# Kernel optimization log

Measured on AMD Instinct MI355X. Metric: run time of the kernel, lower is better.

The kernel has to match this reference:

```python
import jax, jax.numpy as jnp
import numpy as np

N = 6144      # nodes
NFEAT = 512
NHID = 256
NHEADS = 4
DHEAD = NHID // NHEADS  # 64
NEMBED = 128
NEG_INF = -9e15
LRELU_ALPHA = 0.2


def setup_inputs() -> dict:
    key = jax.random.key(0)
    k = jax.random.split(key, 8)
    x = jax.random.normal(k[0], (N, NFEAT), dtype=jnp.float32)
    adj = (jax.random.uniform(k[1], (N, N)) < 0.01).astype(jnp.int32)
    # per-head GAT params, packed over heads
    W = jax.random.normal(k[2], (NHEADS, NFEAT, DHEAD), dtype=jnp.float32) * 0.05
    a_src = jax.random.normal(k[3], (NHEADS, DHEAD), dtype=jnp.float32) * 0.05
    a_dst = jax.random.normal(k[4], (NHEADS, DHEAD), dtype=jnp.float32) * 0.05
    # output linear (init.normal_ std=0.05 per reset_parameters)
    lin_w = jax.random.normal(k[5], (NEMBED, NHID), dtype=jnp.float32) * 0.05
    lin_b = jnp.zeros((NEMBED,), dtype=jnp.float32)
    return {"x": x, "adj": adj, "W": W, "a_src": a_src, "a_dst": a_dst,
            "lin_w": lin_w, "lin_b": lin_b}


def _gat_forward(x, adj, W, a_src, a_dst, lin_w, lin_b):
    # Wh: [H, N, D]
    Wh = jnp.einsum('nf,hfd->hnd', x, W)
    # attention logits e_ij = leakyrelu(a_src.Wh_i + a_dst.Wh_j): [H, N, N]
    s = jnp.einsum('hnd,hd->hn', Wh, a_src)   # source term per node
    t = jnp.einsum('hnd,hd->hn', Wh, a_dst)   # target term per node
    e = s[:, :, None] + t[:, None, :]
    e = jax.nn.leaky_relu(e, negative_slope=LRELU_ALPHA)
    # mask by adjacency, softmax over neighbors
    e = jnp.where(adj[None, :, :] > 0, e, NEG_INF)
    attn = jax.nn.softmax(e, axis=-1)
    # aggregate and per-head ELU (concat=True GAT layer)
    h = jnp.einsum('hnm,hmd->hnd', attn, Wh)
    h = jax.nn.elu(h)
    # concat heads -> [N, NHID]
    h = jnp.transpose(h, (1, 0, 2)).reshape(N, NHID)
    # dropout is identity in eval mode; linear + ELU
    out = jax.nn.elu(h @ lin_w.T + lin_b)
    return out


def reference(x, adj, W, a_src, a_dst, lin_w, lin_b):
    return _gat_forward(x, adj, W, a_src, a_dst, lin_w, lin_b)
```

## Files before the change

### kernel.cpp

```cpp
#include <hip/hip_runtime.h>
#include <hip/hip_bf16.h>
#include <math.h>

#define N_NODES 6144
#define NFEAT 512
#define NHID 256
#define NHEADS 4
#define DHEAD 64
#define NEMBED 128
#define LRELU_ALPHA 0.2f
#define MAXC 256
#define ASTRIDE 20

static __device__ __forceinline__ unsigned short f2bf(float f) {
    unsigned u = __float_as_uint(f);
    unsigned r = (u + 0x7FFFu + ((u >> 16) & 1u)) >> 16;
    return (unsigned short)r;
}

__global__ __launch_bounds__(256) void gemm_scan(const float* __restrict__ x,
                                                 const float* __restrict__ W,
                                                 const float* __restrict__ a_src,
                                                 const float* __restrict__ a_dst,
                                                 const int* __restrict__ adj,
                                                 unsigned short* __restrict__ Whb,
                                                 float* __restrict__ s_arr,
                                                 float* __restrict__ t_arr,
                                                 int* __restrict__ cnt_g,
                                                 unsigned short* __restrict__ nbr_g) {
    __shared__ float As[64][ASTRIDE];
    __shared__ float Bs[16][64];
    const int tid = threadIdx.x;

    if (blockIdx.y < NHEADS) {
        const int tx = tid & 15;
        const int ty = tid >> 4;
        const int row0 = blockIdx.x * 64;
        const int h = blockIdx.y;
        const float* Bp = W + (size_t)h * NFEAT * DHEAD;

        float acc[4][4] = {};

        for (int k0 = 0; k0 < NFEAT; k0 += 16) {
            {
                const int r = tid >> 2, kq = tid & 3;
                const float4 v = *(const float4*)(x + (size_t)(row0 + r) * NFEAT + k0 + kq * 4);
                *(float4*)&As[r][kq * 4] = v;
            }
            {
                const int kk = tid >> 4, cq = tid & 15;
                const float4 v = *(const float4*)(Bp + (size_t)(k0 + kk) * DHEAD + cq * 4);
                *(float4*)&Bs[kk][cq * 4] = v;
            }
            __syncthreads();
#pragma unroll
            for (int kk = 0; kk < 16; kk++) {
                float a[4], b[4];
#pragma unroll
                for (int i = 0; i < 4; i++) a[i] = As[ty * 4 + i][kk];
#pragma unroll
                for (int j = 0; j < 4; j++) b[j] = Bs[kk][tx * 4 + j];
#pragma unroll
                for (int i = 0; i < 4; i++)
#pragma unroll
                    for (int j = 0; j < 4; j++) acc[i][j] += a[i] * b[j];
            }
            __syncthreads();
        }
#pragma unroll
        for (int i = 0; i < 4; i++) {
            const int row = row0 + ty * 4 + i;
            ushort4 w;
            w.x = f2bf(acc[i][0]);
            w.y = f2bf(acc[i][1]);
            w.z = f2bf(acc[i][2]);
            w.w = f2bf(acc[i][3]);
            *(ushort4*)(Whb + ((size_t)h * N_NODES + row) * DHEAD + tx * 4) = w;
        }
        float a4s[4], a4d[4];
#pragma unroll
        for (int j = 0; j < 4; j++) {
            a4s[j] = a_src[h * DHEAD + tx * 4 + j];
            a4d[j] = a_dst[h * DHEAD + tx * 4 + j];
        }
#pragma unroll
        for (int i = 0; i < 4; i++) {
            float ps = acc[i][0] * a4s[0] + acc[i][1] * a4s[1] +
                       acc[i][2] * a4s[2] + acc[i][3] * a4s[3];
            float pt = acc[i][0] * a4d[0] + acc[i][1] * a4d[1] +
                       acc[i][2] * a4d[2] + acc[i][3] * a4d[3];
#pragma unroll
            for (int off = 1; off < 16; off <<= 1) {
                ps += __shfl_xor(ps, off);
                pt += __shfl_xor(pt, off);
            }
            if (tx == 0) {
                const int row = row0 + ty * 4 + i;
                s_arr[h * N_NODES + row] = ps;
                t_arr[h * N_NODES + row] = pt;
            }
        }
    } else {
        const int r = (blockIdx.y - NHEADS) * gridDim.x + blockIdx.x;
        const int* arow = adj + (size_t)r * N_NODES;
        unsigned short* nrow = nbr_g + (size_t)r * MAXC;
        int* cp = cnt_g + r;
#pragma unroll
        for (int it = 0; it < 6; ++it) {
            const int j0 = it * 1024 + tid * 4;
            const int4 v = *(const int4*)(arow + j0);
            const int n = (v.x != 0) + (v.y != 0) + (v.z != 0) + (v.w != 0);
            if (n) {
                int base = atomicAdd(cp, n);
                if (v.x) { if (base < MAXC) nrow[base] = (unsigned short)j0; ++base; }
                if (v.y) { if (base < MAXC) nrow[base] = (unsigned short)(j0 + 1); ++base; }
                if (v.z) { if (base < MAXC) nrow[base] = (unsigned short)(j0 + 2); ++base; }
                if (v.w) { if (base < MAXC) nrow[base] = (unsigned short)(j0 + 3); }
            }
        }
    }
}

__global__ __launch_bounds__(256) void attn_agg(const int* __restrict__ adj,
                                                const unsigned short* __restrict__ Whb,
                                                const float* __restrict__ s_arr,
                                                const float* __restrict__ t_arr,
                                                const int* __restrict__ cnt_g,
                                                const unsigned short* __restrict__ nbr_g,
                                                float* __restrict__ hcat) {
    __shared__ unsigned short nbr[MAXC];
    __shared__ float p_s[NHEADS][MAXC];
    const int i = blockIdx.x;
    const int tid = threadIdx.x;
    const int h = tid >> 6;
    const int lane = tid & 63;
    const int half = lane >> 5;
    const int dp = (lane & 31) * 2;
    const int c = cnt_g[i];
    const unsigned short* wp = Whb + (size_t)h * N_NODES * DHEAD;

    float r0 = 0.0f, r1 = 0.0f, l = 1.0f;
    bool combine = true;
    if (c > 0 && c <= MAXC) {
        for (int k = tid; k < c; k += 256) nbr[k] = nbr_g[(size_t)i * MAXC + k];
        __syncthreads();

        const float s_h = s_arr[h * N_NODES + i];
        const float* tp = t_arr + (size_t)h * N_NODES;
        float m = -INFINITY;
        for (int k = lane; k < c; k += 64) {
            float e = s_h + tp[nbr[k]];
            e = e >= 0.0f ? e : LRELU_ALPHA * e;
            p_s[h][k] = e;
            m = fmaxf(m, e);
        }
#pragma unroll
        for (int off = 32; off > 0; off >>= 1) m = fmaxf(m, __shfl_xor(m, off));
        float ls = 0.0f;
        for (int k = lane; k < c; k += 64) {
            const float p = __expf(p_s[h][k] - m);
            p_s[h][k] = p;
            ls += p;
        }
#pragma unroll
        for (int off = 32; off > 0; off >>= 1) ls += __shfl_xor(ls, off);
        l = ls;

        float ax[8] = {0.f, 0.f, 0.f, 0.f, 0.f, 0.f, 0.f, 0.f};
        float ay[8] = {0.f, 0.f, 0.f, 0.f, 0.f, 0.f, 0.f, 0.f};
        int k = 0;
        for (; k + 16 <= c; k += 16) {
#pragma unroll
            for (int s2 = 0; s2 < 8; ++s2) {
                const int kk = k + 2 * s2 + half;
                const int j = nbr[kk];
                const float p = p_s[h][kk];
                const unsigned w = *(const unsigned*)(wp + (size_t)j * DHEAD + dp);
                ax[s2] += p * __uint_as_float(w << 16);
                ay[s2] += p * __uint_as_float(w & 0xffff0000u);
            }
        }
        for (; k < c; k += 2) {
            const int kk = k + half;
            int j = nbr[k];
            float p = 0.0f;
            if (kk < c) { j = nbr[kk]; p = p_s[h][kk]; }
            const unsigned w = *(const unsigned*)(wp + (size_t)j * DHEAD + dp);
            ax[0] += p * __uint_as_float(w << 16);
            ay[0] += p * __uint_as_float(w & 0xffff0000u);
        }
        r0 = ((ax[0] + ax[1]) + (ax[2] + ax[3])) + ((ax[4] + ax[5]) + (ax[6] + ax[7]));
        r1 = ((ay[0] + ay[1]) + (ay[2] + ay[3])) + ((ay[4] + ay[5]) + (ay[6] + ay[7]));
    } else if (c == 0) {
        for (int j = half; j < N_NODES; j += 2) {
            const unsigned w = *(const unsigned*)(wp + (size_t)j * DHEAD + dp);
            r0 += __uint_as_float(w << 16);
            r1 += __uint_as_float(w & 0xffff0000u);
        }
        l = (float)N_NODES;
    } else {
        combine = false;
        const int* arow = adj + (size_t)i * N_NODES;
        const float s_h = s_arr[h * N_NODES + i];
        const float* tp = t_arr + (size_t)h * N_NODES;
        float m = -INFINITY, ll = 0.0f;
        for (int j = 0; j < N_NODES; j++) {
            if (arow[j]) {
                float e = s_h + tp[j];
                e = e >= 0.0f ? e : LRELU_ALPHA * e;
                const float m_new = fmaxf(m, e);
                const float scale = __expf(m - m_new);
                const float p = __expf(e - m_new);
                ll = ll * scale + p;
                const unsigned w = *(const unsigned*)(wp + (size_t)j * DHEAD + dp);
                r0 = r0 * scale + p * __uint_as_float(w << 16);
                r1 = r1 * scale + p * __uint_as_float(w & 0xffff0000u);
                m = m_new;
            }
        }
        l = ll;
    }
    if (combine) {
        r0 += __shfl_xor(r0, 32);
        r1 += __shfl_xor(r1, 32);
    }
    float hx = r0 / l, hy = r1 / l;
    hx = hx > 0.0f ? hx : expm1f(hx);
    hy = hy > 0.0f ? hy : expm1f(hy);
    if (lane < 32) {
        *(float2*)(hcat + (size_t)i * NHID + h * DHEAD + dp) = make_float2(hx, hy);
    }
}

__global__ __launch_bounds__(256) void out_gemm(const float* __restrict__ hcat,
                                                const float* __restrict__ lin_w,
                                                const float* __restrict__ lin_b,
                                                float* __restrict__ out) {
    __shared__ float As[64][ASTRIDE * 4];
    __shared__ float Bs[16][64];
    const int tid = threadIdx.x;
    const int tx = tid & 15;
    const int ty = tid >> 4;
    const int row0 = blockIdx.x * 64;
    const int c0 = blockIdx.y * 64;

    float acc[4][4] = {};

    for (int k0 = 0; k0 < NHID; k0 += 16) {
        {
            const int r = tid >> 2, kq = tid & 3;
            const float4 v = *(const float4*)(hcat + (size_t)(row0 + r) * NHID + k0 + kq * 4);
            *(float4*)&As[r][kq * 4] = v;
        }
        {
            const int cc = tid & 63, kq = tid >> 6;
            const float4 v = *(const float4*)(lin_w + (size_t)(c0 + cc) * NHID + k0 + kq * 4);
            Bs[kq * 4 + 0][cc] = v.x;
            Bs[kq * 4 + 1][cc] = v.y;
            Bs[kq * 4 + 2][cc] = v.z;
            Bs[kq * 4 + 3][cc] = v.w;
        }
        __syncthreads();
#pragma unroll
        for (int kk = 0; kk < 16; kk++) {
            float a[4], b[4];
#pragma unroll
            for (int i = 0; i < 4; i++) a[i] = As[ty * 4 + i][kk];
#pragma unroll
            for (int j = 0; j < 4; j++) b[j] = Bs[kk][tx * 4 + j];
#pragma unroll
            for (int i = 0; i < 4; i++)
#pragma unroll
                for (int j = 0; j < 4; j++) acc[i][j] += a[i] * b[j];
        }
        __syncthreads();
    }
#pragma unroll
    for (int i = 0; i < 4; i++) {
        const int row = row0 + ty * 4 + i;
        float v[4];
#pragma unroll
        for (int j = 0; j < 4; j++) {
            const int col = c0 + tx * 4 + j;
            float val = acc[i][j] + lin_b[col];
            v[j] = val > 0.0f ? val : expm1f(val);
        }
        *(float4*)(out + (size_t)row * NEMBED + c0 + tx * 4) =
            make_float4(v[0], v[1], v[2], v[3]);
    }
}

extern "C" void kernel_launch(void* const* d_in, const int* in_sizes, int n_in,
                              void* d_out, int out_size, void* d_ws, size_t ws_size,
                              hipStream_t stream) {
    const float* x     = (const float*)d_in[0];
    const int*   adj   = (const int*)d_in[1];
    const float* W     = (const float*)d_in[2];
    const float* a_src = (const float*)d_in[3];
    const float* a_dst = (const float*)d_in[4];
    const float* lin_w = (const float*)d_in[5];
    const float* lin_b = (const float*)d_in[6];
    float* out = (float*)d_out;

    unsigned short* Whb = (unsigned short*)d_ws;
    float* s    = (float*)(Whb + (size_t)NHEADS * N_NODES * DHEAD);
    float* t    = s + (size_t)NHEADS * N_NODES;
    float* hcat = t + (size_t)NHEADS * N_NODES;
    int* cnt_g  = (int*)(hcat + (size_t)N_NODES * NHID);
    unsigned short* nbr_g = (unsigned short*)(cnt_g + N_NODES);

    hipMemsetAsync(cnt_g, 0, N_NODES * sizeof(int), stream);
    gemm_scan<<<dim3(96, NHEADS + 64), 256, 0, stream>>>(
        x, W, a_src, a_dst, adj, Whb, s, t, cnt_g, nbr_g);
    attn_agg<<<N_NODES, 256, 0, stream>>>(adj, Whb, s, t, cnt_g, nbr_g, hcat);
    out_gemm<<<dim3(N_NODES / 64, NEMBED / 64), 256, 0, stream>>>(hcat, lin_w, lin_b, out);
}
```

Measured before the change: 277.9 us.

## Fuse output linear into attention kernel and count neighbors in LDS

The output linear layer plus ELU is folded into the per-node attention kernel. Each block writes its concatenated hidden row to shared memory and computes the 128 outputs with wave-level dot products against lin_w. This removes the hcat round trip through global memory and one kernel launch. The neighbor scan now counts in a shared-memory atomic and writes the count once, which drops the memset and the global atomics. Aggregation now uses 8-byte bf16 loads with four neighbors in flight per wave. The cost is that every block rereads lin_w (128 KB) from cache, and a serial per-row dot-product loop is added.

```diff
diff --git a/kernel.cpp b/kernel.cpp
--- a/kernel.cpp
+++ b/kernel.cpp
@@ -17,6 +17,8 @@
     unsigned r = (u + 0x7FFFu + ((u >> 16) & 1u)) >> 16;
     return (unsigned short)r;
 }
+static __device__ __forceinline__ float bfLo(unsigned u) { return __uint_as_float(u << 16); }
+static __device__ __forceinline__ float bfHi(unsigned u) { return __uint_as_float(u & 0xffff0000u); }
 
 __global__ __launch_bounds__(256) void gemm_scan(const float* __restrict__ x,
                                                  const float* __restrict__ W,
@@ -30,6 +32,7 @@
                                                  unsigned short* __restrict__ nbr_g) {
     __shared__ float As[64][ASTRIDE];
     __shared__ float Bs[16][64];
+    __shared__ int scnt;
     const int tid = threadIdx.x;
 
     if (blockIdx.y < NHEADS) {
@@ -104,43 +107,52 @@
         const int r = (blockIdx.y - NHEADS) * gridDim.x + blockIdx.x;
         const int* arow = adj + (size_t)r * N_NODES;
         unsigned short* nrow = nbr_g + (size_t)r * MAXC;
-        int* cp = cnt_g + r;
+        if (tid == 0) scnt = 0;
+        __syncthreads();
 #pragma unroll
         for (int it = 0; it < 6; ++it) {
             const int j0 = it * 1024 + tid * 4;
             const int4 v = *(const int4*)(arow + j0);
             const int n = (v.x != 0) + (v.y != 0) + (v.z != 0) + (v.w != 0);
             if (n) {
-                int base = atomicAdd(cp, n);
+                int base = atomicAdd(&scnt, n);
                 if (v.x) { if (base < MAXC) nrow[base] = (unsigned short)j0; ++base; }
                 if (v.y) { if (base < MAXC) nrow[base] = (unsigned short)(j0 + 1); ++base; }
                 if (v.z) { if (base < MAXC) nrow[base] = (unsigned short)(j0 + 2); ++base; }
                 if (v.w) { if (base < MAXC) nrow[base] = (unsigned short)(j0 + 3); }
             }
         }
+        __syncthreads();
+        if (tid == 0) cnt_g[r] = scnt;
     }
 }
 
-__global__ __launch_bounds__(256) void attn_agg(const int* __restrict__ adj,
+__global__ __launch_bounds__(256) void attn_out(const int* __restrict__ adj,
                                                 const unsigned short* __restrict__ Whb,
                                                 const float* __restrict__ s_arr,
                                                 const float* __restrict__ t_arr,
                                                 const int* __restrict__ cnt_g,
                                                 const unsigned short* __restrict__ nbr_g,
-                                                float* __restrict__ hcat) {
+                                                const float* __restrict__ lin_w,
+                                                const float* __restrict__ lin_b,
+                                                float* __restrict__ out) {
     __shared__ unsigned short nbr[MAXC];
     __shared__ float p_s[NHEADS][MAXC];
+    __shared__ float hrow[NHID];
+    __shared__ float part[NEMBED];
     const int i = blockIdx.x;
     const int tid = threadIdx.x;
     const int h = tid >> 6;
     const int lane = tid & 63;
-    const int half = lane >> 5;
-    const int dp = (lane & 31) * 2;
+    const int q = lane >> 4;
+    const int dq = (lane & 15) * 4;
     const int c = cnt_g[i];
     const unsigned short* wp = Whb + (size_t)h * N_NODES * DHEAD;
 
-    float r0 = 0.0f, r1 = 0.0f, l = 1.0f;
+    float b0[4] = {0.f, 0.f, 0.f, 0.f};
+    float l = 1.0f;
     bool combine = true;
+
     if (c > 0 && c <= MAXC) {
         for (int k = tid; k < c; k += 256) nbr[k] = nbr_g[(size_t)i * MAXC + k];
         __syncthreads();
@@ -166,36 +178,43 @@
         for (int off = 32; off > 0; off >>= 1) ls += __shfl_xor(ls, off);
         l = ls;
 
-        float ax[8] = {0.f, 0.f, 0.f, 0.f, 0.f, 0.f, 0.f, 0.f};
-        float ay[8] = {0.f, 0.f, 0.f, 0.f, 0.f, 0.f, 0.f, 0.f};
+        float b1[4] = {0.f, 0.f, 0.f, 0.f};
+        float b2[4] = {0.f, 0.f, 0.f, 0.f};
+        float b3[4] = {0.f, 0.f, 0.f, 0.f};
         int k = 0;
         for (; k + 16 <= c; k += 16) {
-#pragma unroll
-            for (int s2 = 0; s2 < 8; ++s2) {
-                const int kk = k + 2 * s2 + half;
-                const int j = nbr[kk];
-                const float p = p_s[h][kk];
-                const unsigned w = *(const unsigned*)(wp + (size_t)j * DHEAD + dp);
-                ax[s2] += p * __uint_as_float(w << 16);
-                ay[s2] += p * __uint_as_float(w & 0xffff0000u);
-            }
-        }
-        for (; k < c; k += 2) {
-            const int kk = k + half;
-            int j = nbr[k];
-            float p = 0.0f;
-            if (kk < c) { j = nbr[kk]; p = p_s[h][kk]; }
-            const unsigned w = *(const unsigned*)(wp + (size_t)j * DHEAD + dp);
-            ax[0] += p * __uint_as_float(w << 16);
-            ay[0] += p * __uint_as_float(w & 0xffff0000u);
-        }
-        r0 = ((ax[0] + ax[1]) + (ax[2] + ax[3])) + ((ax[4] + ax[5]) + (ax[6] + ax[7]));
-        r1 = ((ay[0] + ay[1]) + (ay[2] + ay[3])) + ((ay[4] + ay[5]) + (ay[6] + ay[7]));
+            const int k0 = k + q, k1 = k + 4 + q, k2 = k + 8 + q, k3 = k + 12 + q;
+            const int j0 = nbr[k0], j1 = nbr[k1], j2 = nbr[k2], j3 = nbr[k3];
+            const float p0 = p_s[h][k0], p1 = p_s[h][k1];
+            const float p2 = p_s[h][k2], p3 = p_s[h][k3];
+            const uint2 w0 = *(const uint2*)(wp + (size_t)j0 * DHEAD + dq);
+            const uint2 w1 = *(const uint2*)(wp + (size_t)j1 * DHEAD + dq);
+            const uint2 w2 = *(const uint2*)(wp + (size_t)j2 * DHEAD + dq);
+            const uint2 w3 = *(const uint2*)(wp + (size_t)j3 * DHEAD + dq);
+            b0[0] += p0 * bfLo(w0.x); b0[1] += p0 * bfHi(w0.x);
+            b0[2] += p0 * bfLo(w0.y); b0[3] += p0 * bfHi(w0.y);
+            b1[0] += p1 * bfLo(w1.x); b1[1] += p1 * bfHi(w1.x);
+            b1[2] += p1 * bfLo(w1.y); b1[3] += p1 * bfHi(w1.y);
+            b2[0] += p2 * bfLo(w2.x); b2[1] += p2 * bfHi(w2.x);
+            b2[2] += p2 * bfLo(w2.y); b2[3] += p2 * bfHi(w2.y);
+            b3[0] += p3 * bfLo(w3.x); b3[1] += p3 * bfHi(w3.x);
+            b3[2] += p3 * bfLo(w3.y); b3[3] += p3 * bfHi(w3.y);
+        }
+        for (; k < c; k += 4) {
+            const int kk = k + q;
+            const int j = (kk < c) ? nbr[kk] : nbr[k];
+            const float p = (kk < c) ? p_s[h][kk] : 0.0f;
+            const uint2 w = *(const uint2*)(wp + (size_t)j * DHEAD + dq);
+            b0[0] += p * bfLo(w.x); b0[1] += p * bfHi(w.x);
+            b0[2] += p * bfLo(w.y); b0[3] += p * bfHi(w.y);
+        }
+#pragma unroll
+        for (int d = 0; d < 4; d++) b0[d] = (b0[d] + b1[d]) + (b2[d] + b3[d]);
     } else if (c == 0) {
-        for (int j = half; j < N_NODES; j += 2) {
-            const unsigned w = *(const unsigned*)(wp + (size_t)j * DHEAD + dp);
-            r0 += __uint_as_float(w << 16);
-            r1 += __uint_as_float(w & 0xffff0000u);
+        for (int j = q; j < N_NODES; j += 4) {
+            const uint2 w = *(const uint2*)(wp + (size_t)j * DHEAD + dq);
+            b0[0] += bfLo(w.x); b0[1] += bfHi(w.x);
+            b0[2] += bfLo(w.y); b0[3] += bfHi(w.y);
         }
         l = (float)N_NODES;
     } else {
@@ -212,82 +231,49 @@
                 const float scale = __expf(m - m_new);
                 const float p = __expf(e - m_new);
                 ll = ll * scale + p;
-                const unsigned w = *(const unsigned*)(wp + (size_t)j * DHEAD + dp);
-                r0 = r0 * scale + p * __uint_as_float(w << 16);
-                r1 = r1 * scale + p * __uint_as_float(w & 0xffff0000u);
+                const uint2 w = *(const uint2*)(wp + (size_t)j * DHEAD + dq);
+                b0[0] = b0[0] * scale + p * bfLo(w.x);
+                b0[1] = b0[1] * scale + p * bfHi(w.x);
+                b0[2] = b0[2] * scale + p * bfLo(w.y);
+                b0[3] = b0[3] * scale + p * bfHi(w.y);
                 m = m_new;
             }
         }
         l = ll;
     }
+
     if (combine) {
-        r0 += __shfl_xor(r0, 32);
-        r1 += __shfl_xor(r1, 32);
-    }
-    float hx = r0 / l, hy = r1 / l;
-    hx = hx > 0.0f ? hx : expm1f(hx);
-    hy = hy > 0.0f ? hy : expm1f(hy);
-    if (lane < 32) {
-        *(float2*)(hcat + (size_t)i * NHID + h * DHEAD + dp) = make_float2(hx, hy);
-    }
-}
-
-__global__ __launch_bounds__(256) void out_gemm(const float* __restrict__ hcat,
-                                                const float* __restrict__ lin_w,
-                                                const float* __restrict__ lin_b,
-                                                float* __restrict__ out) {
-    __shared__ float As[64][ASTRIDE * 4];
-    __shared__ float Bs[16][64];
-    const int tid = threadIdx.x;
-    const int tx = tid & 15;
-    const int ty = tid >> 4;
-    const int row0 = blockIdx.x * 64;
-    const int c0 = blockIdx.y * 64;
-
-    float acc[4][4] = {};
-
-    for (int k0 = 0; k0 < NHID; k0 += 16) {
-        {
-            const int r = tid >> 2, kq = tid & 3;
-            const float4 v = *(const float4*)(hcat + (size_t)(row0 + r) * NHID + k0 + kq * 4);
-            *(float4*)&As[r][kq * 4] = v;
-        }
-        {
-            const int cc = tid & 63, kq = tid >> 6;
-            const float4 v = *(const float4*)(lin_w + (size_t)(c0 + cc) * NHID + k0 + kq * 4);
-            Bs[kq * 4 + 0][cc] = v.x;
-            Bs[kq * 4 + 1][cc] = v.y;
-            Bs[kq * 4 + 2][cc] = v.z;
-            Bs[kq * 4 + 3][cc] = v.w;
-        }
-        __syncthreads();
-#pragma unroll
-        for (int kk = 0; kk < 16; kk++) {
-            float a[4], b[4];
-#pragma unroll
-            for (int i = 0; i < 4; i++) a[i] = As[ty * 4 + i][kk];
-#pragma unroll
-            for (int j = 0; j < 4; j++) b[j] = Bs[kk][tx * 4 + j];
-#pragma unroll
-            for (int i = 0; i < 4; i++)
-#pragma unroll
-                for (int j = 0; j < 4; j++) acc[i][j] += a[i] * b[j];
-        }
-        __syncthreads();
-    }
-#pragma unroll
-    for (int i = 0; i < 4; i++) {
-        const int row = row0 + ty * 4 + i;
-        float v[4];
-#pragma unroll
-        for (int j = 0; j < 4; j++) {
-            const int col = c0 + tx * 4 + j;
-            float val = acc[i][j] + lin_b[col];
-            v[j] = val > 0.0f ? val : expm1f(val);
-        }
-        *(float4*)(out + (size_t)row * NEMBED + c0 + tx * 4) =
-            make_float4(v[0], v[1], v[2], v[3]);
-    }
+#pragma unroll
+        for (int d = 0; d < 4; d++) {
+            b0[d] += __shfl_xor(b0[d], 16);
+            b0[d] += __shfl_xor(b0[d], 32);
+        }
+    }
+    if (lane < 16) {
+        float4 hv;
+        float* pv = &hv.x;
+#pragma unroll
+        for (int d = 0; d < 4; d++) {
+            float v = b0[d] / l;
+            pv[d] = v > 0.0f ? v : expm1f(v);
+        }
+        *(float4*)&hrow[h * DHEAD + dq] = hv;
+    }
+    __syncthreads();
+
+    const float4 hb = *(const float4*)&hrow[lane * 4];
+    for (int j = h; j < NEMBED; j += NHEADS) {
+        const float4 wv = *(const float4*)(lin_w + (size_t)j * NHID + lane * 4);
+        float d = wv.x * hb.x + wv.y * hb.y + wv.z * hb.z + wv.w * hb.w;
+#pragma unroll
+        for (int off = 32; off > 0; off >>= 1) d += __shfl_xor(d, off);
+        if (lane == 0) {
+            float val = d + lin_b[j];
+            part[j] = val > 0.0f ? val : expm1f(val);
+        }
+    }
+    __syncthreads();
+    if (tid < NEMBED) out[(size_t)i * NEMBED + tid] = part[tid];
 }
 
 extern "C" void kernel_launch(void* const* d_in, const int* in_sizes, int n_in,
@@ -305,13 +291,11 @@
     unsigned short* Whb = (unsigned short*)d_ws;
     float* s    = (float*)(Whb + (size_t)NHEADS * N_NODES * DHEAD);
     float* t    = s + (size_t)NHEADS * N_NODES;
-    float* hcat = t + (size_t)NHEADS * N_NODES;
-    int* cnt_g  = (int*)(hcat + (size_t)N_NODES * NHID);
+    int* cnt_g  = (int*)(t + (size_t)NHEADS * N_NODES);
     unsigned short* nbr_g = (unsigned short*)(cnt_g + N_NODES);
 
-    hipMemsetAsync(cnt_g, 0, N_NODES * sizeof(int), stream);
     gemm_scan<<<dim3(96, NHEADS + 64), 256, 0, stream>>>(
         x, W, a_src, a_dst, adj, Whb, s, t, cnt_g, nbr_g);
-    attn_agg<<<N_NODES, 256, 0, stream>>>(adj, Whb, s, t, cnt_g, nbr_g, hcat);
-    out_gemm<<<dim3(N_NODES / 64, NEMBED / 64), 256, 0, stream>>>(hcat, lin_w, lin_b, out);
+    attn_out<<<N_NODES, 256, 0, stream>>>(adj, Whb, s, t, cnt_g, nbr_g,
+                                          lin_w, lin_b, out);
 }
```

After: 322.2 us. 15.9% more time.
